# Kernel optimization log

Hardware: AMD Instinct MI355X
Metric: run time of the kernel (lower is better)

## Reference

```python
import jax, jax.numpy as jnp
import numpy as np

V, D, H, KH, FF, E = 50257, 512, 8, 64, 2048, 4
B, S = 8, 1024


def _glorot(key, shape):
    # VarianceScaling(1.0, 'fan_avg') with normal-ish draw
    fan_in, fan_out = shape[-2], shape[-1]
    scale = np.sqrt(2.0 / (fan_in + fan_out)).astype(np.float32)
    return jax.random.normal(key, shape, dtype=jnp.float32) * scale


def _mha(x, Wq, Wk, Wv, Wo):
    # haiku MultiHeadAttention (self-attn, no mask, zero biases at init)
    b, s, _ = x.shape
    q = (x @ Wq).reshape(b, s, H, KH)
    k = (x @ Wk).reshape(b, s, H, KH)
    v = (x @ Wv).reshape(b, s, H, KH)
    logits = jnp.einsum('bthd,bThd->bhtT', q, k) / jnp.asarray(np.sqrt(KH), x.dtype)
    attn = jax.nn.softmax(logits, axis=-1)
    o = jnp.einsum('bhtT,bThd->bthd', attn, v).reshape(b, s, H * KH)
    return o @ Wo


def setup_inputs() -> dict:
    key = jax.random.key(0)
    ks = jax.random.split(key, 16)
    tokens = jax.random.randint(ks[0], (B, S), 0, V, dtype=jnp.int32)
    emb = jax.random.normal(ks[1], (V, D), dtype=jnp.float32) * 0.02
    Wq = _glorot(ks[2], (D, H * KH))
    Wk = _glorot(ks[3], (D, H * KH))
    Wv = _glorot(ks[4], (D, H * KH))
    Wo = _glorot(ks[5], (H * KH, D))
    W1 = _glorot(ks[6], (D, FF))
    W2 = _glorot(ks[7], (FF, D))
    Wg = _glorot(ks[8], (D, E))
    eWq = _glorot(ks[9], (E, D, H * KH))
    eWk = _glorot(ks[10], (E, D, H * KH))
    eWv = _glorot(ks[11], (E, D, H * KH))
    eWo = _glorot(ks[12], (E, H * KH, D))
    eW1 = _glorot(ks[13], (E, D, FF))
    eW2 = _glorot(ks[14], (E, FF, D))
    Wout = _glorot(ks[15], (D, 1))
    return dict(tokens=tokens, emb=emb, Wq=Wq, Wk=Wk, Wv=Wv, Wo=Wo, W1=W1, W2=W2,
                Wg=Wg, eWq=eWq, eWk=eWk, eWv=eWv, eWo=eWo, eW1=eW1, eW2=eW2, Wout=Wout)


def reference(tokens, emb, Wq, Wk, Wv, Wo, W1, W2, Wg, eWq, eWk, eWv, eWo, eW1, eW2, Wout):
    x = emb[tokens]                                     # [B,S,D] embedding gather
    h = (_mha(x, Wq, Wk, Wv, Wo) @ W1) @ W2             # shared transformer block
    gate = h @ Wg                                       # [B,S,E]
    idx = jnp.argmax(gate, axis=-1)                     # [B,S] per-token expert id
    out = jnp.zeros_like(h)
    for e in range(E):                                  # naive masked dense dispatch
        mask = (idx == e)[..., None]                    # [B,S,1]
        xe = jnp.where(mask, h, 0.0)
        ye = (_mha(xe, eWq[e], eWk[e], eWv[e], eWo[e]) @ eW1[e]) @ eW2[e]
        out = out + ye                                  # sum-aggregate expert outputs
    return out @ Wout                                   # [B,S,1]
```

## Files before the change

kernel.cpp:

```cpp
#include <hip/hip_runtime.h>
#include <stdint.h>
#include <stddef.h>

typedef __bf16 bf16_8 __attribute__((ext_vector_type(8)));
typedef float  f32x4  __attribute__((ext_vector_type(4)));

__device__ __forceinline__ unsigned short f2bf(float f) {
    unsigned u = __float_as_uint(f);
    unsigned r = (u + 0x7fffu + ((u >> 16) & 1u)) >> 16;
    return (unsigned short)r;
}
__device__ __forceinline__ float bf2f(unsigned short s) {
    return __uint_as_float(((unsigned)s) << 16);
}
__device__ __forceinline__ void split3(float v, unsigned short& h, unsigned short& l, unsigned short& l2) {
    h = f2bf(v);
    float r1 = v - bf2f(h);
    l = f2bf(r1);
    l2 = f2bf(r1 - bf2f(l));
}
__device__ __forceinline__ void split2(float v, unsigned short& h, unsigned short& l) {
    h = f2bf(v);
    l = f2bf(v - bf2f(h));
}

template<int P>
__global__ __launch_bounds__(256)
void wsplit_kernel(const float* __restrict__ s0, const float* __restrict__ s1,
                   const float* __restrict__ s2, const float* __restrict__ s3,
                   unsigned short* __restrict__ d0, unsigned short* __restrict__ d1,
                   unsigned short* __restrict__ d2, unsigned short* __restrict__ d3,
                   int K, int N, int nper, size_t sstride, size_t dstride)
{
    const int z = blockIdx.z;
    const int arr = z / nper, e = z - arr * nper;
    const float* src = (arr == 0 ? s0 : arr == 1 ? s1 : arr == 2 ? s2 : s3) + (size_t)e * sstride;
    unsigned short* dst = (arr == 0 ? d0 : arr == 1 ? d1 : arr == 2 ? d2 : d3) + (size_t)e * dstride;
    const size_t NK = (size_t)N * K;
    __shared__ float T[64][65];
    const int n0 = blockIdx.x * 64, k0 = blockIdx.y * 64;
    const int tid = threadIdx.x;
#pragma unroll
    for (int i = 0; i < 16; ++i) {
        int idx = tid + (i << 8);
        int kk = idx >> 6, nn = idx & 63;
        T[kk][nn] = src[(size_t)(k0 + kk) * N + n0 + nn];
    }
    __syncthreads();
#pragma unroll
    for (int i = 0; i < 4; ++i) {
        int idx = (tid + (i << 8)) << 2;
        int nn = idx >> 6, kk = idx & 63;
        ushort4 hv, lv, l2v;
        unsigned short* hp = (unsigned short*)&hv;
        unsigned short* lp = (unsigned short*)&lv;
        unsigned short* l2p = (unsigned short*)&l2v;
#pragma unroll
        for (int j = 0; j < 4; ++j) {
            float v = T[kk + j][nn];
            unsigned short h = f2bf(v);
            hp[j] = h;
            if (P == 3) {
                float r1 = v - bf2f(h);
                unsigned short l = f2bf(r1);
                lp[j] = l;
                l2p[j] = f2bf(r1 - bf2f(l));
            }
        }
        unsigned short* dp = dst + (size_t)(n0 + nn) * K + k0 + kk;
        *(ushort4*)dp = hv;
        if (P == 3) {
            *(ushort4*)(dp + NK) = lv;
            *(ushort4*)(dp + 2 * NK) = l2v;
        }
    }
}

template<int TERMS, int AMODE, int CMODE, int NW, int BPRE, int A16, int C16>
__global__ __launch_bounds__(256, 2)
void gemm_kernel(const void* __restrict__ Av,
                 const void* __restrict__ B0, const void* __restrict__ B1, const void* __restrict__ B2,
                 void* __restrict__ C0, void* __restrict__ C1, void* __restrict__ C2,
                 int M, int N, int K,
                 size_t astride, size_t bstride, size_t cstride,
                 const int* __restrict__ OFF, const int* __restrict__ flat)
{
    const int z = blockIdx.z;
    const int e = z / NW, w = z - e * NW;
    int base = 0, cnt = M;
    if (AMODE == 1 || AMODE == 2 || CMODE == 1 || CMODE == 2) {
        base = OFF[e * 8];
        cnt  = OFF[e * 8 + 8] - base;
        if ((int)blockIdx.x * 128 >= cnt) return;
    }
    const void* Bsel = (NW == 3 ? (w == 0 ? B0 : w == 1 ? B1 : B2) : B0);
    void*       Csel = (NW == 3 ? (w == 0 ? C0 : w == 1 ? C1 : C2) : C0);
    const float*          Af = (const float*)Av + (size_t)e * astride;
    const unsigned short* As = (const unsigned short*)Av;
    const float*          Bf = (const float*)Bsel + (size_t)e * bstride;
    const unsigned short* Bp = (const unsigned short*)Bsel + (size_t)e * bstride;
    float*          Cf = (float*)Csel + (size_t)e * cstride;
    unsigned short* Cs = (unsigned short*)Csel + (size_t)e * cstride;
    const size_t NKb = (size_t)N * K;

    constexpr int NPL = (TERMS == 6) ? 3 : 1;
    __shared__ unsigned short Asm[NPL][128 * 40];
    __shared__ unsigned short Bsm[NPL][128 * 40];

    const int tid   = threadIdx.x;
    const int lane  = tid & 63;
    const int wid   = tid >> 6;
    const int wm    = wid & 1, wn = wid >> 1;
    const int mlane = lane & 15, quad = lane >> 4;
    const int row0  = blockIdx.x * 128;
    const int col0  = blockIdx.y * 128;

    f32x4 acc[4][4];
#pragma unroll
    for (int i = 0; i < 4; ++i)
#pragma unroll
        for (int j = 0; j < 4; ++j)
#pragma unroll
            for (int r = 0; r < 4; ++r) acc[i][j][r] = 0.f;

    for (int k0 = 0; k0 < K; k0 += 32) {
        if (A16 == 0) {
#pragma unroll
            for (int i = 0; i < 4; ++i) {
                int idx = tid + (i << 8);
                int r = idx >> 3;
                int c = (idx & 7) << 2;
                int lr = row0 + r;
                if (AMODE != 0) lr = min(lr, cnt - 1);
                size_t arow = (AMODE == 2) ? (size_t)flat[base + lr]
                            : (AMODE == 1) ? (size_t)(base + lr) : (size_t)lr;
                const float4 a = *(const float4*)(Af + arow * K + k0 + c);
                float av[4] = {a.x, a.y, a.z, a.w};
                ushort4 hv, lv, l2v;
                unsigned short* hp  = (unsigned short*)&hv;
                unsigned short* lp  = (unsigned short*)&lv;
                unsigned short* l2p = (unsigned short*)&l2v;
#pragma unroll
                for (int j = 0; j < 4; ++j) {
                    unsigned short h = f2bf(av[j]);
                    hp[j] = h;
                    if (TERMS == 6) {
                        float r1 = av[j] - bf2f(h);
                        unsigned short l = f2bf(r1);
                        lp[j]  = l;
                        l2p[j] = f2bf(r1 - bf2f(l));
                    }
                }
                *(ushort4*)&Asm[0][r * 40 + c] = hv;
                if (TERMS == 6) {
                    *(ushort4*)&Asm[1][r * 40 + c] = lv;
                    *(ushort4*)&Asm[2][r * 40 + c] = l2v;
                }
            }
        } else {
#pragma unroll
            for (int p = 0; p < NPL; ++p)
#pragma unroll
                for (int j = 0; j < 2; ++j) {
                    int c = tid * 2 + j;
                    int r = c >> 2, q8 = (c & 3) << 3;
                    int lr = row0 + r;
                    if (AMODE != 0) lr = min(lr, cnt - 1);
                    size_t arow = (AMODE == 2) ? (size_t)flat[base + lr]
                                : (AMODE == 1) ? (size_t)(base + lr) : (size_t)lr;
                    *(uint4*)&Asm[p][r * 40 + q8] =
                        *(const uint4*)(As + (size_t)p * astride + arow * K + k0 + q8);
                }
        }
        if (BPRE == 0) {
#pragma unroll
            for (int i = 0; i < 2; ++i) {
                int idx = tid + (i << 8);
                int kk = idx >> 4;
                int n8 = (idx & 15) << 3;
                const float* bp = Bf + (size_t)(k0 + kk) * N + col0 + n8;
                const float4 b0 = *(const float4*)bp;
                const float4 b1 = *(const float4*)(bp + 4);
                float bv[8] = {b0.x, b0.y, b0.z, b0.w, b1.x, b1.y, b1.z, b1.w};
#pragma unroll
                for (int j = 0; j < 8; ++j) {
                    unsigned short h = f2bf(bv[j]);
                    Bsm[0][(n8 + j) * 40 + kk] = h;
                    if (TERMS == 6) {
                        float r1 = bv[j] - bf2f(h);
                        unsigned short l = f2bf(r1);
                        Bsm[1][(n8 + j) * 40 + kk] = l;
                        Bsm[2][(n8 + j) * 40 + kk] = f2bf(r1 - bf2f(l));
                    }
                }
            }
        } else {
#pragma unroll
            for (int p = 0; p < NPL; ++p)
#pragma unroll
                for (int j = 0; j < 2; ++j) {
                    int c = tid * 2 + j;
                    int r = c >> 2, q8 = (c & 3) << 3;
                    *(uint4*)&Bsm[p][r * 40 + q8] =
                        *(const uint4*)(Bp + (size_t)p * NKb + (size_t)(col0 + r) * K + k0 + q8);
                }
        }
        __syncthreads();

        bf16_8 fa[3][4], fb[3][4];
#pragma unroll
        for (int t = 0; t < 4; ++t) {
            int ar = (wm * 64 + t * 16 + mlane) * 40 + quad * 8;
            int br = (wn * 64 + t * 16 + mlane) * 40 + quad * 8;
            fa[0][t] = *(const bf16_8*)&Asm[0][ar];
            fb[0][t] = *(const bf16_8*)&Bsm[0][br];
            if (TERMS == 6) {
                fa[1][t] = *(const bf16_8*)&Asm[1][ar];
                fa[2][t] = *(const bf16_8*)&Asm[2][ar];
                fb[1][t] = *(const bf16_8*)&Bsm[1][br];
                fb[2][t] = *(const bf16_8*)&Bsm[2][br];
            }
        }
        const int ta[6] = {0, 0, 1, 0, 1, 2};
        const int tb[6] = {0, 1, 0, 2, 1, 0};
#pragma unroll
        for (int s = 0; s < TERMS; ++s)
#pragma unroll
            for (int mt = 0; mt < 4; ++mt)
#pragma unroll
                for (int nt = 0; nt < 4; ++nt)
                    acc[mt][nt] = __builtin_amdgcn_mfma_f32_16x16x32_bf16(
                        fa[ta[s]][mt], fb[tb[s]][nt], acc[mt][nt], 0, 0, 0);
        __syncthreads();
    }

#pragma unroll
    for (int mt = 0; mt < 4; ++mt)
#pragma unroll
        for (int nt = 0; nt < 4; ++nt) {
            int c = col0 + wn * 64 + nt * 16 + mlane;
#pragma unroll
            for (int j = 0; j < 4; ++j) {
                int lr = row0 + wm * 64 + mt * 16 + quad * 4 + j;
                if ((CMODE == 1 || CMODE == 2) && lr >= cnt) continue;
                size_t crow = (CMODE == 2) ? (size_t)flat[base + lr]
                            : (CMODE == 1) ? (size_t)(base + lr) : (size_t)lr;
                if (C16) Cs[crow * N + c] = f2bf(acc[mt][nt][j]);
                else     Cf[crow * N + c] = acc[mt][nt][j];
            }
        }
}

__global__ __launch_bounds__(256)
void meanv_gemm_kernel(const float* __restrict__ in, const float* __restrict__ W,
                       float* __restrict__ out, int N, int K,
                       size_t instride, size_t wstride, size_t outstride)
{
    const int e  = blockIdx.z;
    const int nl = threadIdx.x & 63;
    const int kg = threadIdx.x >> 6;
    const int n  = blockIdx.x * 64 + nl;
    const int k0 = blockIdx.y * 512;

    const float* inp = in + (size_t)e * instride + k0;
    const float* wp  = W + (size_t)e * wstride + (size_t)(k0 + kg * 128) * N + n;

    __shared__ float mv[8][512];
    for (int i = threadIdx.x; i < 4096; i += 256) {
        int b = i >> 9, k = i & 511;
        mv[b][k] = inp[(size_t)b * K + k];
    }
    __syncthreads();

    float acc[8] = {0.f, 0.f, 0.f, 0.f, 0.f, 0.f, 0.f, 0.f};
#pragma unroll 8
    for (int k = 0; k < 128; ++k) {
        float wv = wp[(size_t)k * N];
        const float* mk = &mv[0][kg * 128 + k];
#pragma unroll
        for (int b = 0; b < 8; ++b) acc[b] += mk[b * 512] * wv;
    }

    __shared__ float red[4][8][64];
#pragma unroll
    for (int b = 0; b < 8; ++b) red[kg][b][nl] = acc[b];
    __syncthreads();
    if (kg == 0) {
        float* op = out + (size_t)e * outstride + n;
#pragma unroll
        for (int b = 0; b < 8; ++b) {
            float s = red[0][b][nl] + red[1][b][nl] + red[2][b][nl] + red[3][b][nl];
            if (gridDim.y == 1) op[(size_t)b * N] = s;
            else                atomicAdd(&op[(size_t)b * N], s);
        }
    }
}

__global__ __launch_bounds__(256, 2)
void attn_kernel(const float* __restrict__ Q, const float* __restrict__ Km,
                 const float* __restrict__ V, float* __restrict__ O)
{
    __shared__ __align__(16) unsigned short Ks[3][2][32][40];
    __shared__ __align__(16) unsigned short Vt[3][64][40];
    __shared__ __align__(16) unsigned short U[15360];

    const int tid = threadIdx.x;
    const int lane = tid & 63;
    const int w = tid >> 6;
    const int mlane = lane & 15, quad = lane >> 4;

    const int qt = blockIdx.x & 15;
    const int h  = (blockIdx.x >> 4) & 7;
    const int b  = blockIdx.x >> 7;
    const size_t rowbase = (size_t)b * 1024;
    const int colbase = h * 64;

#pragma unroll
    for (int i = 0; i < 4; ++i) {
        int idx = tid + (i << 8);
        int r = idx >> 4, c4 = (idx & 15) << 2;
        const float4 a = *(const float4*)(Q + (rowbase + qt * 64 + r) * 512 + colbase + c4);
        float av[4] = {a.x, a.y, a.z, a.w};
        ushort4 hv, lv, l2v;
        unsigned short* hp  = (unsigned short*)&hv;
        unsigned short* lp  = (unsigned short*)&lv;
        unsigned short* l2p = (unsigned short*)&l2v;
#pragma unroll
        for (int j = 0; j < 4; ++j) split3(av[j], hp[j], lp[j], l2p[j]);
        int ch = c4 >> 5, cm = c4 & 31;
        *(ushort4*)&U[(((0 * 2 + ch) * 64) + r) * 40 + cm] = hv;
        *(ushort4*)&U[(((1 * 2 + ch) * 64) + r) * 40 + cm] = lv;
        *(ushort4*)&U[(((2 * 2 + ch) * 64) + r) * 40 + cm] = l2v;
    }
    __syncthreads();

    bf16_8 fq[3][2];
#pragma unroll
    for (int p = 0; p < 3; ++p)
#pragma unroll
        for (int c = 0; c < 2; ++c)
            fq[p][c] = *(const bf16_8*)&U[(((p * 2 + c) * 64) + (w * 16 + mlane)) * 40 + quad * 8];
    __syncthreads();

    f32x4 oacc[4];
#pragma unroll
    for (int i = 0; i < 4; ++i)
#pragma unroll
        for (int j = 0; j < 4; ++j) oacc[i][j] = 0.f;
    float m_run = -1e30f, l_run = 0.f;

    const int ta[6] = {0, 0, 1, 0, 1, 2};
    const int tb[6] = {0, 1, 0, 2, 1, 0};

    for (int tt = 0; tt < 32; ++tt) {
        __syncthreads();
#pragma unroll
        for (int i = 0; i < 2; ++i) {
            int idx = tid + (i << 8);
            int r = idx >> 4, c4 = (idx & 15) << 2;
            const float4 a = *(const float4*)(Km + (rowbase + tt * 32 + r) * 512 + colbase + c4);
            float av[4] = {a.x, a.y, a.z, a.w};
            ushort4 hv, lv, l2v;
            unsigned short* hp  = (unsigned short*)&hv;
            unsigned short* lp  = (unsigned short*)&lv;
            unsigned short* l2p = (unsigned short*)&l2v;
#pragma unroll
            for (int j = 0; j < 4; ++j) split3(av[j], hp[j], lp[j], l2p[j]);
            int ch = c4 >> 5, cm = c4 & 31;
            *(ushort4*)&Ks[0][ch][r][cm] = hv;
            *(ushort4*)&Ks[1][ch][r][cm] = lv;
            *(ushort4*)&Ks[2][ch][r][cm] = l2v;
        }
#pragma unroll
        for (int i = 0; i < 2; ++i) {
            int idx = tid + (i << 8);
            int d = idx & 63, k4 = (idx >> 6) << 2;
            const float* vp = V + (rowbase + tt * 32 + k4) * 512 + colbase + d;
            float vv[4] = {vp[0], vp[512], vp[1024], vp[1536]};
            ushort4 hv, lv, l2v;
            unsigned short* hp  = (unsigned short*)&hv;
            unsigned short* lp  = (unsigned short*)&lv;
            unsigned short* l2p = (unsigned short*)&l2v;
#pragma unroll
            for (int j = 0; j < 4; ++j) split3(vv[j], hp[j], lp[j], l2p[j]);
            *(ushort4*)&Vt[0][d][k4] = hv;
            *(ushort4*)&Vt[1][d][k4] = lv;
            *(ushort4*)&Vt[2][d][k4] = l2v;
        }
        __syncthreads();

        f32x4 sacc[2];
#pragma unroll
        for (int mm = 0; mm < 2; ++mm)
#pragma unroll
            for (int j = 0; j < 4; ++j) sacc[mm][j] = 0.f;
        bf16_8 fk[3][2][2];
#pragma unroll
        for (int p = 0; p < 3; ++p)
#pragma unroll
            for (int c = 0; c < 2; ++c)
#pragma unroll
                for (int mm = 0; mm < 2; ++mm)
                    fk[p][c][mm] = *(const bf16_8*)&Ks[p][c][mm * 16 + mlane][quad * 8];
#pragma unroll
        for (int s = 0; s < 6; ++s)
#pragma unroll
            for (int c = 0; c < 2; ++c)
#pragma unroll
                for (int mm = 0; mm < 2; ++mm)
                    sacc[mm] = __builtin_amdgcn_mfma_f32_16x16x32_bf16(
                        fk[ta[s]][c][mm], fq[tb[s]][c], sacc[mm], 0, 0, 0);

        float sv[2][4];
#pragma unroll
        for (int mm = 0; mm < 2; ++mm)
#pragma unroll
            for (int j = 0; j < 4; ++j) sv[mm][j] = sacc[mm][j] * 0.125f;
        float tmax = sv[0][0];
#pragma unroll
        for (int mm = 0; mm < 2; ++mm)
#pragma unroll
            for (int j = 0; j < 4; ++j) tmax = fmaxf(tmax, sv[mm][j]);
        tmax = fmaxf(tmax, __shfl_xor(tmax, 16));
        tmax = fmaxf(tmax, __shfl_xor(tmax, 32));
        float mnew = fmaxf(m_run, tmax);
        float alpha = __expf(m_run - mnew);
        float lsum = 0.f;
#pragma unroll
        for (int mm = 0; mm < 2; ++mm)
#pragma unroll
            for (int j = 0; j < 4; ++j) {
                float p = __expf(sv[mm][j] - mnew);
                sv[mm][j] = p;
                lsum += p;
            }
        lsum += __shfl_xor(lsum, 16);
        lsum += __shfl_xor(lsum, 32);
        l_run = l_run * alpha + lsum;
        m_run = mnew;
#pragma unroll
        for (int mm = 0; mm < 4; ++mm)
#pragma unroll
            for (int j = 0; j < 4; ++j) oacc[mm][j] *= alpha;

#pragma unroll
        for (int mm = 0; mm < 2; ++mm) {
            ushort4 hv, lv, l2v;
            unsigned short* hp  = (unsigned short*)&hv;
            unsigned short* lp  = (unsigned short*)&lv;
            unsigned short* l2p = (unsigned short*)&l2v;
#pragma unroll
            for (int j = 0; j < 4; ++j) split3(sv[mm][j], hp[j], lp[j], l2p[j]);
            int col = mm * 16 + quad * 4;
            *(ushort4*)&U[((w * 3 + 0) * 16 + mlane) * 40 + col] = hv;
            *(ushort4*)&U[((w * 3 + 1) * 16 + mlane) * 40 + col] = lv;
            *(ushort4*)&U[((w * 3 + 2) * 16 + mlane) * 40 + col] = l2v;
        }

        bf16_8 fp[3], fv[3][4];
#pragma unroll
        for (int p = 0; p < 3; ++p) {
            fp[p] = *(const bf16_8*)&U[((w * 3 + p) * 16 + mlane) * 40 + quad * 8];
#pragma unroll
            for (int mm = 0; mm < 4; ++mm)
                fv[p][mm] = *(const bf16_8*)&Vt[p][mm * 16 + mlane][quad * 8];
        }
#pragma unroll
        for (int s = 0; s < 6; ++s)
#pragma unroll
            for (int mm = 0; mm < 4; ++mm)
                oacc[mm] = __builtin_amdgcn_mfma_f32_16x16x32_bf16(
                    fv[ta[s]][mm], fp[tb[s]], oacc[mm], 0, 0, 0);
    }

    const float inv = 1.f / l_run;
    const size_t orow = (rowbase + qt * 64 + w * 16 + mlane) * 512 + colbase;
#pragma unroll
    for (int mm = 0; mm < 4; ++mm)
#pragma unroll
        for (int j = 0; j < 4; ++j)
            O[orow + mm * 16 + quad * 4 + j] = oacc[mm][j] * inv;
}

__global__ __launch_bounds__(256, 3)
void attn_compact_kernel(const float* __restrict__ Qc, const float* __restrict__ Kc,
                         const float* __restrict__ Vc, const float* __restrict__ meanV,
                         unsigned short* __restrict__ AOc, const int* __restrict__ OFF)
{
    const int qt = blockIdx.x & 15;
    const int h  = (blockIdx.x >> 4) & 7;
    const int e  = (blockIdx.x >> 7) & 3;
    const int b  = blockIdx.x >> 9;
    const int base = OFF[e * 8 + b];
    const int c    = OFF[e * 8 + b + 1] - base;
    if (qt * 64 >= c) return;
    const int nq = min(64, c - qt * 64);

    __shared__ __align__(16) unsigned short Ks[2][2][32][40];
    __shared__ __align__(16) unsigned short Vt[2][64][40];
    __shared__ __align__(16) unsigned short U[10240];

    const int tid = threadIdx.x;
    const int lane = tid & 63;
    const int w = tid >> 6;
    const int mlane = lane & 15, quad = lane >> 4;
    const int colbase = h * 64;
    const int cmax = c - 1;

#pragma unroll
    for (int i = 0; i < 4; ++i) {
        int idx = tid + (i << 8);
        int r = idx >> 4, c4 = (idx & 15) << 2;
        const size_t g = (size_t)(base + min(qt * 64 + r, cmax)) * 512 + colbase + c4;
        const float4 a = *(const float4*)(Qc + g);
        float av[4] = {a.x, a.y, a.z, a.w};
        ushort4 hv, lv;
        unsigned short* hp = (unsigned short*)&hv;
        unsigned short* lp = (unsigned short*)&lv;
#pragma unroll
        for (int j = 0; j < 4; ++j) split2(av[j], hp[j], lp[j]);
        int ch = c4 >> 5, cm = c4 & 31;
        *(ushort4*)&U[(((0 * 2 + ch) * 64) + r) * 40 + cm] = hv;
        *(ushort4*)&U[(((1 * 2 + ch) * 64) + r) * 40 + cm] = lv;
    }
    __syncthreads();

    bf16_8 fq[2][2];
#pragma unroll
    for (int p = 0; p < 2; ++p)
#pragma unroll
        for (int cc = 0; cc < 2; ++cc)
            fq[p][cc] = *(const bf16_8*)&U[(((p * 2 + cc) * 64) + (w * 16 + mlane)) * 40 + quad * 8];
    __syncthreads();

    f32x4 oacc[4];
#pragma unroll
    for (int i = 0; i < 4; ++i)
#pragma unroll
        for (int j = 0; j < 4; ++j) oacc[i][j] = 0.f;
    float m_run = -1e30f, l_run = 0.f;

    const int ta3[3] = {0, 0, 1};
    const int tb3[3] = {0, 1, 0};

    for (int kt = 0; kt * 32 < c; ++kt) {
        __syncthreads();
#pragma unroll
        for (int i = 0; i < 2; ++i) {
            int idx = tid + (i << 8);
            int r = idx >> 4, c4 = (idx & 15) << 2;
            const size_t g = (size_t)(base + min(kt * 32 + r, cmax)) * 512 + colbase + c4;
            const float4 a = *(const float4*)(Kc + g);
            float av[4] = {a.x, a.y, a.z, a.w};
            ushort4 hv, lv;
            unsigned short* hp = (unsigned short*)&hv;
            unsigned short* lp = (unsigned short*)&lv;
#pragma unroll
            for (int j = 0; j < 4; ++j) split2(av[j], hp[j], lp[j]);
            int ch = c4 >> 5, cm = c4 & 31;
            *(ushort4*)&Ks[0][ch][r][cm] = hv;
            *(ushort4*)&Ks[1][ch][r][cm] = lv;
        }
#pragma unroll
        for (int i = 0; i < 2; ++i) {
            int idx = tid + (i << 8);
            int d = idx & 63, k4 = (idx >> 6) << 2;
            float vv[4];
#pragma unroll
            for (int j = 0; j < 4; ++j)
                vv[j] = Vc[(size_t)(base + min(kt * 32 + k4 + j, cmax)) * 512 + colbase + d];
            ushort4 hv, lv;
            unsigned short* hp = (unsigned short*)&hv;
            unsigned short* lp = (unsigned short*)&lv;
#pragma unroll
            for (int j = 0; j < 4; ++j) split2(vv[j], hp[j], lp[j]);
            *(ushort4*)&Vt[0][d][k4] = hv;
            *(ushort4*)&Vt[1][d][k4] = lv;
        }
        __syncthreads();

        f32x4 sacc[2];
#pragma unroll
        for (int mm = 0; mm < 2; ++mm)
#pragma unroll
            for (int j = 0; j < 4; ++j) sacc[mm][j] = 0.f;
        bf16_8 fk[2][2][2];
#pragma unroll
        for (int p = 0; p < 2; ++p)
#pragma unroll
            for (int cc = 0; cc < 2; ++cc)
#pragma unroll
                for (int mm = 0; mm < 2; ++mm)
                    fk[p][cc][mm] = *(const bf16_8*)&Ks[p][cc][mm * 16 + mlane][quad * 8];
#pragma unroll
        for (int s = 0; s < 3; ++s)
#pragma unroll
            for (int cc = 0; cc < 2; ++cc)
#pragma unroll
                for (int mm = 0; mm < 2; ++mm)
                    sacc[mm] = __builtin_amdgcn_mfma_f32_16x16x32_bf16(
                        fk[ta3[s]][cc][mm], fq[tb3[s]][cc], sacc[mm], 0, 0, 0);

        float sv[2][4];
#pragma unroll
        for (int mm = 0; mm < 2; ++mm)
#pragma unroll
            for (int j = 0; j < 4; ++j) {
                int kg = kt * 32 + mm * 16 + quad * 4 + j;
                sv[mm][j] = (kg < c) ? sacc[mm][j] * 0.125f : -1e30f;
            }
        float tmax = sv[0][0];
#pragma unroll
        for (int mm = 0; mm < 2; ++mm)
#pragma unroll
            for (int j = 0; j < 4; ++j) tmax = fmaxf(tmax, sv[mm][j]);
        tmax = fmaxf(tmax, __shfl_xor(tmax, 16));
        tmax = fmaxf(tmax, __shfl_xor(tmax, 32));
        float mnew = fmaxf(m_run, tmax);
        float alpha = __expf(m_run - mnew);
        float lsum = 0.f;
#pragma unroll
        for (int mm = 0; mm < 2; ++mm)
#pragma unroll
            for (int j = 0; j < 4; ++j) {
                float p = __expf(sv[mm][j] - mnew);
                sv[mm][j] = p;
                lsum += p;
            }
        lsum += __shfl_xor(lsum, 16);
        lsum += __shfl_xor(lsum, 32);
        l_run = l_run * alpha + lsum;
        m_run = mnew;
#pragma unroll
        for (int mm = 0; mm < 4; ++mm)
#pragma unroll
            for (int j = 0; j < 4; ++j) oacc[mm][j] *= alpha;

#pragma unroll
        for (int mm = 0; mm < 2; ++mm) {
            ushort4 hv, lv;
            unsigned short* hp = (unsigned short*)&hv;
            unsigned short* lp = (unsigned short*)&lv;
#pragma unroll
            for (int j = 0; j < 4; ++j) split2(sv[mm][j], hp[j], lp[j]);
            int col = mm * 16 + quad * 4;
            *(ushort4*)&U[((w * 2 + 0) * 16 + mlane) * 40 + col] = hv;
            *(ushort4*)&U[((w * 2 + 1) * 16 + mlane) * 40 + col] = lv;
        }

        bf16_8 fp[2], fv[2][4];
#pragma unroll
        for (int p = 0; p < 2; ++p) {
            fp[p] = *(const bf16_8*)&U[((w * 2 + p) * 16 + mlane) * 40 + quad * 8];
#pragma unroll
            for (int mm = 0; mm < 4; ++mm)
                fv[p][mm] = *(const bf16_8*)&Vt[p][mm * 16 + mlane][quad * 8];
        }
#pragma unroll
        for (int s = 0; s < 3; ++s)
#pragma unroll
            for (int mm = 0; mm < 4; ++mm)
                oacc[mm] = __builtin_amdgcn_mfma_f32_16x16x32_bf16(
                    fv[ta3[s]][mm], fp[tb3[s]], oacc[mm], 0, 0, 0);
    }

    float mfin = (c < 1024) ? fmaxf(m_run, 0.f) : m_run;
    float alphaf = __expf(m_run - mfin);
    l_run = l_run * alphaf + (float)(1024 - c) * __expf(-mfin);
#pragma unroll
    for (int mm = 0; mm < 4; ++mm)
#pragma unroll
        for (int j = 0; j < 4; ++j) oacc[mm][j] *= alphaf;

    const int qi = w * 16 + mlane;
    if (qi < nq) {
        const float inv = 1.f / l_run;
        const size_t orow = (size_t)(base + qt * 64 + qi) * 512 + colbase;
        const float* mv = meanV + e * 65536 + b * 512 + colbase;
#pragma unroll
        for (int mm = 0; mm < 4; ++mm) {
            int d0 = mm * 16 + quad * 4;
            ushort4 o;
            o.x = f2bf(oacc[mm][0] * inv - mv[d0 + 0]);
            o.y = f2bf(oacc[mm][1] * inv - mv[d0 + 1]);
            o.z = f2bf(oacc[mm][2] * inv - mv[d0 + 2]);
            o.w = f2bf(oacc[mm][3] * inv - mv[d0 + 3]);
            *(ushort4*)&AOc[orow + d0] = o;
        }
    }
}

__global__ void sumv_kernel(const float* __restrict__ Vc, const int* __restrict__ OFF,
                            float* __restrict__ M32)
{
    const int h = blockIdx.x & 7, e = (blockIdx.x >> 3) & 3, b = blockIdx.x >> 5;
    const int base = OFF[e * 8 + b], c = OFF[e * 8 + b + 1] - base;
    const int tid = threadIdx.x;
    const int d = tid & 63, g = tid >> 6;
    float s = 0.f;
    for (int r = g; r < c; r += 4) s += Vc[(size_t)(base + r) * 512 + h * 64 + d];
    __shared__ float red[256];
    red[tid] = s;
    __syncthreads();
    if (g == 0)
        M32[e * 65536 + b * 512 + h * 64 + d] =
            (red[d] + red[64 + d] + red[128 + d] + red[192 + d]) * (1.f / 1024.f);
}

__global__ void gather_kernel(const int* __restrict__ tokens,
                              const float* __restrict__ emb,
                              unsigned short* __restrict__ Xp)
{
    const int t = blockIdx.x;
    const int tok = tokens[t];
    const int d4 = threadIdx.x * 4;
    const float4 a = *(const float4*)(emb + (size_t)tok * 512 + d4);
    float av[4] = {a.x, a.y, a.z, a.w};
    ushort4 hv, lv, l2v;
    unsigned short* hp  = (unsigned short*)&hv;
    unsigned short* lp  = (unsigned short*)&lv;
    unsigned short* l2p = (unsigned short*)&l2v;
#pragma unroll
    for (int j = 0; j < 4; ++j) split3(av[j], hp[j], lp[j], l2p[j]);
    const size_t o = (size_t)t * 512 + d4;
    *(ushort4*)&Xp[o]           = hv;
    *(ushort4*)&Xp[o + 4194304] = lv;
    *(ushort4*)&Xp[o + 8388608] = l2v;
}

__global__ __launch_bounds__(256)
void gate_kernel(const float* __restrict__ H, const float* __restrict__ Wg,
                 int* __restrict__ idx)
{
    const int t = blockIdx.x * 4 + (threadIdx.x >> 6);
    const int lane = threadIdx.x & 63;
    float a0 = 0, a1 = 0, a2 = 0, a3 = 0;
#pragma unroll
    for (int i = 0; i < 8; ++i) {
        int d = i * 64 + lane;
        float hv = H[(size_t)t * 512 + d];
        a0 += hv * Wg[d * 4 + 0];
        a1 += hv * Wg[d * 4 + 1];
        a2 += hv * Wg[d * 4 + 2];
        a3 += hv * Wg[d * 4 + 3];
    }
#pragma unroll
    for (int off = 32; off > 0; off >>= 1) {
        a0 += __shfl_down(a0, off);
        a1 += __shfl_down(a1, off);
        a2 += __shfl_down(a2, off);
        a3 += __shfl_down(a3, off);
    }
    if (lane == 0) {
        int best = 0; float bv = a0;
        if (a1 > bv) { bv = a1; best = 1; }
        if (a2 > bv) { bv = a2; best = 2; }
        if (a3 > bv) { bv = a3; best = 3; }
        idx[t] = best;
    }
}

__global__ void count_kernel(const int* __restrict__ idx, int* __restrict__ cnt)
{
    const int t = blockIdx.x * 256 + threadIdx.x;
    atomicAdd(&cnt[idx[t] * 8 + (t >> 10)], 1);
}
__global__ void offsets_kernel(const int* __restrict__ cnt, int* __restrict__ OFF,
                               int* __restrict__ cursor)
{
    if (threadIdx.x == 0) {
        int a = 0;
        for (int i = 0; i < 32; ++i) { OFF[i] = a; cursor[i] = a; a += cnt[i]; }
        OFF[32] = a;
    }
}
__global__ void fill_kernel(const int* __restrict__ idx, int* __restrict__ cursor,
                            int* __restrict__ flat)
{
    const int t = blockIdx.x * 256 + threadIdx.x;
    const int p = atomicAdd(&cursor[idx[t] * 8 + (t >> 10)], 1);
    flat[p] = t;
}

__global__ void sb_kernel(const float* __restrict__ G2, const float* __restrict__ Wout,
                          float* __restrict__ SB)
{
    const int tid = threadIdx.x;
    const int pair = tid >> 3, t8 = tid & 7;
    const int e = pair >> 3, b = pair & 7;
    float s = 0.f;
    for (int d = t8; d < 512; d += 8) s += G2[e * 65536 + b * 512 + d] * Wout[d];
    __shared__ float red[256];
    __shared__ float red2[32];
    red[tid] = s;
    __syncthreads();
    if (tid < 32) {
        float t = 0.f;
#pragma unroll
        for (int k = 0; k < 8; ++k) t += red[tid * 8 + k];
        red2[tid] = t;
    }
    __syncthreads();
    if (tid < 8)
        SB[tid] = red2[tid] + red2[8 + tid] + red2[16 + tid] + red2[24 + tid];
}

__global__ __launch_bounds__(256)
void wout_kernel(const float* __restrict__ OUT, const float* __restrict__ Wout,
                 const float* __restrict__ SB, float* __restrict__ out)
{
    const int t = blockIdx.x * 4 + (threadIdx.x >> 6);
    const int lane = threadIdx.x & 63;
    float s = 0.f;
#pragma unroll
    for (int i = 0; i < 8; ++i) {
        int d = i * 64 + lane;
        s += OUT[(size_t)t * 512 + d] * Wout[d];
    }
#pragma unroll
    for (int off = 32; off > 0; off >>= 1) s += __shfl_down(s, off);
    if (lane == 0) out[t] = s + SB[t >> 10];
}

extern "C" void kernel_launch(void* const* d_in, const int* in_sizes, int n_in,
                              void* d_out, int out_size, void* d_ws, size_t ws_size,
                              hipStream_t stream)
{
    const int*   tokens = (const int*)d_in[0];
    const float* emb  = (const float*)d_in[1];
    const float* Wq   = (const float*)d_in[2];
    const float* Wk   = (const float*)d_in[3];
    const float* Wv   = (const float*)d_in[4];
    const float* Wo   = (const float*)d_in[5];
    const float* W1   = (const float*)d_in[6];
    const float* W2   = (const float*)d_in[7];
    const float* Wg   = (const float*)d_in[8];
    const float* eWq  = (const float*)d_in[9];
    const float* eWk  = (const float*)d_in[10];
    const float* eWv  = (const float*)d_in[11];
    const float* eWo  = (const float*)d_in[12];
    const float* eW1  = (const float*)d_in[13];
    const float* eW2  = (const float*)d_in[14];
    const float* Wout = (const float*)d_in[15];
    float* outp = (float*)d_out;

    float* WS = (float*)d_ws;
    const size_t SZ = (size_t)8192 * 512;
    float* P0 = WS, *P1 = WS + SZ, *P2 = WS + 2 * SZ, *P3 = WS + 3 * SZ, *P4 = WS + 4 * SZ;

    unsigned short* SP   = (unsigned short*)(WS + 5 * SZ);
    unsigned short* sW1p = SP;
    unsigned short* sW2p = SP + 3145728;
    unsigned short* xWq  = SP + 6291456;
    unsigned short* xWk  = xWq + 1048576;
    unsigned short* xWv  = xWk + 1048576;
    unsigned short* xWo  = xWv + 1048576;
    unsigned short* xW1  = xWo + 1048576;
    unsigned short* xW2  = xW1 + 4194304;

    float* MBase = WS + 5 * SZ + 9437184;
    int* IDX    = (int*)MBase;
    int* cnt    = (int*)(MBase + 8192);
    int* OFFp   = (int*)(MBase + 8224);
    int* cursor = (int*)(MBase + 8264);
    int* flat   = (int*)(MBase + 8304);
    float* M32  = MBase + 16640;
    float* G0   = M32 + 262144;
    float* G2   = G0 + 262144;
    float* SB   = G2 + 262144;

    float* Qb = P0, *Kb = P1, *Vb = P2, *AO = P3, *T0 = P4, *T1 = P0, *Hb = P4;
    unsigned short* Xp = (unsigned short*)P3;
    float* Qc = P0, *Kc = P1, *Vc = P2;
    unsigned short* AOc = (unsigned short*)P3;
    unsigned short* T0c = (unsigned short*)(P3 + 2097152);
    unsigned short* T1c = (unsigned short*)P0;
    float* G1 = P2;
    float* OA = P3;

    const int M = 8192, D = 512, FF = 2048;
    const size_t sDD = (size_t)D * D, sDF = (size_t)D * FF;
    const float* NUL = nullptr;
    float* NULm = nullptr;

    wsplit_kernel<3><<<dim3(32, 8, 1),  256, 0, stream>>>(W1, NUL, NUL, NUL, sW1p, 0, 0, 0, D, FF, 1, 0, 0);
    wsplit_kernel<3><<<dim3(8, 32, 1),  256, 0, stream>>>(W2, NUL, NUL, NUL, sW2p, 0, 0, 0, FF, D, 1, 0, 0);
    wsplit_kernel<3><<<dim3(8, 8, 4),   256, 0, stream>>>(Wq, Wk, Wv, Wo, xWq, xWk, xWv, xWo, D, D, 1, 0, 0);
    wsplit_kernel<1><<<dim3(32, 8, 4),  256, 0, stream>>>(eW1, NUL, NUL, NUL, xW1, 0, 0, 0, D, FF, 4, sDF, 1048576);
    wsplit_kernel<1><<<dim3(8, 32, 4),  256, 0, stream>>>(eW2, NUL, NUL, NUL, xW2, 0, 0, 0, FF, D, 4, sDF, 1048576);

    gather_kernel<<<8192, 128, 0, stream>>>(tokens, emb, Xp);
    gemm_kernel<6, 0, 0, 3, 1, 1, 0><<<dim3(64, 4, 3), 256, 0, stream>>>(
        Xp, xWq, xWk, xWv, Qb, Kb, Vb, M, D, D, (size_t)M * D, 0, 0, nullptr, nullptr);
    attn_kernel<<<1024, 256, 0, stream>>>(Qb, Kb, Vb, AO);
    gemm_kernel<6, 0, 0, 1, 1, 0, 0><<<dim3(64, 4, 1), 256, 0, stream>>>(
        AO, xWo, NUL, NUL, T0, NULm, NULm, M, D, D, 0, 0, 0, nullptr, nullptr);
    wsplit_kernel<1><<<dim3(8, 8, 16),  256, 0, stream>>>(eWq, eWk, eWv, eWo, xWq, xWk, xWv, xWo, D, D, 4, sDD, 262144);
    gemm_kernel<6, 0, 0, 1, 1, 0, 0><<<dim3(64, 16, 1), 256, 0, stream>>>(
        T0, sW1p, NUL, NUL, T1, NULm, NULm, M, FF, D, 0, 0, 0, nullptr, nullptr);
    gemm_kernel<6, 0, 0, 1, 1, 0, 0><<<dim3(64, 4, 1), 256, 0, stream>>>(
        T1, sW2p, NUL, NUL, Hb, NULm, NULm, M, D, FF, 0, 0, 0, nullptr, nullptr);
    gate_kernel<<<2048, 256, 0, stream>>>(Hb, Wg, IDX);

    hipMemsetAsync(cnt, 0, 32 * sizeof(int), stream);
    hipMemsetAsync(M32, 0, 4 * 128 * 512 * sizeof(float), stream);
    hipMemsetAsync(G2, 0, 262144 * sizeof(float), stream);
    count_kernel<<<32, 256, 0, stream>>>(IDX, cnt);
    offsets_kernel<<<1, 64, 0, stream>>>(cnt, OFFp, cursor);
    fill_kernel<<<32, 256, 0, stream>>>(IDX, cursor, flat);

    gemm_kernel<1, 2, 1, 3, 1, 0, 0><<<dim3(64, 4, 12), 256, 0, stream>>>(
        Hb, xWq, xWk, xWv, Qc, Kc, Vc, M, D, D, 0, 262144, 0, OFFp, flat);
    sumv_kernel<<<256, 256, 0, stream>>>(Vc, OFFp, M32);
    attn_compact_kernel<<<4096, 256, 0, stream>>>(Qc, Kc, Vc, M32, AOc, OFFp);

    gemm_kernel<1, 1, 1, 1, 1, 1, 1><<<dim3(64, 4, 4), 256, 0, stream>>>(
        AOc, xWo, NUL, NUL, T0c, NULm, NULm, M, D, D, 0, 262144, 0, OFFp, flat);
    gemm_kernel<1, 1, 1, 1, 1, 1, 1><<<dim3(64, 16, 4), 256, 0, stream>>>(
        T0c, xW1, NUL, NUL, T1c, NULm, NULm, M, FF, D, 0, 1048576, 0, OFFp, flat);

    meanv_gemm_kernel<<<dim3(8, 1, 4),  256, 0, stream>>>(M32, eWo, G0, 512,  512,  65536,  sDD, 65536);
    meanv_gemm_kernel<<<dim3(32, 1, 4), 256, 0, stream>>>(G0,  eW1, G1, 2048, 512,  65536,  sDF, 262144);
    meanv_gemm_kernel<<<dim3(8, 4, 4),  256, 0, stream>>>(G1,  eW2, G2, 512,  2048, 262144, sDF, 65536);

    gemm_kernel<1, 1, 2, 1, 1, 1, 0><<<dim3(64, 4, 4), 256, 0, stream>>>(
        T1c, xW2, NUL, NUL, OA, NULm, NULm, M, D, FF, 0, 1048576, 0, OFFp, flat);

    sb_kernel<<<1, 256, 0, stream>>>(G2, Wout, SB);
    wout_kernel<<<2048, 256, 0, stream>>>(OA, Wout, SB, outp);
}
```

Baseline: 1.384 ms.

## Emit pre-split bf16 K/V planes from GEMM epilogues instead of splitting in attention

The Q/K/V projection GEMMs are split into separate launches, and the K and V ones now write bf16 hi/lo(/lo2) planes directly in their epilogue (new C16 modes 2 and 3). The attention kernels then load ready-made bf16 planes into shared memory and no longer run the split arithmetic once per query-tile block. This removes the redundant split work repeated across query tiles. In exchange it costs three GEMM launches instead of one, more global bytes per plane, and strided 16-bit V loads. Some weight-split launches are also moved later in the sequence.

```diff
diff --git a/kernel.cpp b/kernel.cpp
--- a/kernel.cpp
+++ b/kernel.cpp
@@ -101,6 +101,7 @@
     const unsigned short* Bp = (const unsigned short*)Bsel + (size_t)e * bstride;
     float*          Cf = (float*)Csel + (size_t)e * cstride;
     unsigned short* Cs = (unsigned short*)Csel + (size_t)e * cstride;
+    unsigned short* Cp = (unsigned short*)Csel;
     const size_t NKb = (size_t)N * K;
 
     constexpr int NPL = (TERMS == 6) ? 3 : 1;
@@ -245,8 +246,20 @@
                 if ((CMODE == 1 || CMODE == 2) && lr >= cnt) continue;
                 size_t crow = (CMODE == 2) ? (size_t)flat[base + lr]
                             : (CMODE == 1) ? (size_t)(base + lr) : (size_t)lr;
-                if (C16) Cs[crow * N + c] = f2bf(acc[mt][nt][j]);
-                else     Cf[crow * N + c] = acc[mt][nt][j];
+                size_t o = crow * N + c;
+                if (C16 == 2) {
+                    unsigned short h, l, l2;
+                    split3(acc[mt][nt][j], h, l, l2);
+                    Cp[o] = h; Cp[cstride + o] = l; Cp[2 * cstride + o] = l2;
+                } else if (C16 == 3) {
+                    unsigned short h, l;
+                    split2(acc[mt][nt][j], h, l);
+                    Cp[o] = h; Cp[cstride + o] = l;
+                } else if (C16 == 1) {
+                    Cs[o] = f2bf(acc[mt][nt][j]);
+                } else {
+                    Cf[o] = acc[mt][nt][j];
+                }
             }
         }
 }
@@ -297,8 +310,8 @@
 }
 
 __global__ __launch_bounds__(256, 2)
-void attn_kernel(const float* __restrict__ Q, const float* __restrict__ Km,
-                 const float* __restrict__ V, float* __restrict__ O)
+void attn_kernel(const float* __restrict__ Q, const unsigned short* __restrict__ Kp,
+                 const unsigned short* __restrict__ Vp, float* __restrict__ O)
 {
     __shared__ __align__(16) unsigned short Ks[3][2][32][40];
     __shared__ __align__(16) unsigned short Vt[3][64][40];
@@ -352,40 +365,29 @@
     const int ta[6] = {0, 0, 1, 0, 1, 2};
     const int tb[6] = {0, 1, 0, 2, 1, 0};
 
+    const int kr = tid >> 3, kc8 = (tid & 7) << 3;
+    const int kch = kc8 >> 5, kcm = kc8 & 31;
+
     for (int tt = 0; tt < 32; ++tt) {
         __syncthreads();
+        {
+            const size_t g = (rowbase + tt * 32 + kr) * 512 + colbase + kc8;
+#pragma unroll
+            for (int p = 0; p < 3; ++p)
+                *(uint4*)&Ks[p][kch][kr][kcm] = *(const uint4*)(Kp + (size_t)p * 4194304 + g);
+        }
 #pragma unroll
         for (int i = 0; i < 2; ++i) {
             int idx = tid + (i << 8);
-            int r = idx >> 4, c4 = (idx & 15) << 2;
-            const float4 a = *(const float4*)(Km + (rowbase + tt * 32 + r) * 512 + colbase + c4);
-            float av[4] = {a.x, a.y, a.z, a.w};
-            ushort4 hv, lv, l2v;
-            unsigned short* hp  = (unsigned short*)&hv;
-            unsigned short* lp  = (unsigned short*)&lv;
-            unsigned short* l2p = (unsigned short*)&l2v;
-#pragma unroll
-            for (int j = 0; j < 4; ++j) split3(av[j], hp[j], lp[j], l2p[j]);
-            int ch = c4 >> 5, cm = c4 & 31;
-            *(ushort4*)&Ks[0][ch][r][cm] = hv;
-            *(ushort4*)&Ks[1][ch][r][cm] = lv;
-            *(ushort4*)&Ks[2][ch][r][cm] = l2v;
-        }
-#pragma unroll
-        for (int i = 0; i < 2; ++i) {
-            int idx = tid + (i << 8);
-            int d = idx & 63, k4 = (idx >> 6) << 2;
-            const float* vp = V + (rowbase + tt * 32 + k4) * 512 + colbase + d;
-            float vv[4] = {vp[0], vp[512], vp[1024], vp[1536]};
-            ushort4 hv, lv, l2v;
-            unsigned short* hp  = (unsigned short*)&hv;
-            unsigned short* lp  = (unsigned short*)&lv;
-            unsigned short* l2p = (unsigned short*)&l2v;
-#pragma unroll
-            for (int j = 0; j < 4; ++j) split3(vv[j], hp[j], lp[j], l2p[j]);
-            *(ushort4*)&Vt[0][d][k4] = hv;
-            *(ushort4*)&Vt[1][d][k4] = lv;
-            *(ushort4*)&Vt[2][d][k4] = l2v;
+            int vd = idx & 63, vk4 = (idx >> 6) << 2;
+            const size_t g = (rowbase + tt * 32 + vk4) * 512 + colbase + vd;
+#pragma unroll
+            for (int p = 0; p < 3; ++p) {
+                const unsigned short* vp = Vp + (size_t)p * 16777216 + g;
+                ushort4 vv;
+                vv.x = vp[0]; vv.y = vp[512]; vv.z = vp[1024]; vv.w = vp[1536];
+                *(ushort4*)&Vt[p][vd][vk4] = vv;
+            }
         }
         __syncthreads();
 
@@ -483,8 +485,8 @@
 }
 
 __global__ __launch_bounds__(256, 3)
-void attn_compact_kernel(const float* __restrict__ Qc, const float* __restrict__ Kc,
-                         const float* __restrict__ Vc, const float* __restrict__ meanV,
+void attn_compact_kernel(const float* __restrict__ Qc, const unsigned short* __restrict__ Kc,
+                         const unsigned short* __restrict__ Vc, const float* __restrict__ meanV,
                          unsigned short* __restrict__ AOc, const int* __restrict__ OFF)
 {
     const int qt = blockIdx.x & 15;
@@ -543,39 +545,31 @@
     const int ta3[3] = {0, 0, 1};
     const int tb3[3] = {0, 1, 0};
 
+    const int kr = tid >> 3, kc8 = (tid & 7) << 3;
+    const int kch = kc8 >> 5, kcm = kc8 & 31;
+
     for (int kt = 0; kt * 32 < c; ++kt) {
         __syncthreads();
+        {
+            const size_t g = (size_t)(base + min(kt * 32 + kr, cmax)) * 512 + colbase + kc8;
+#pragma unroll
+            for (int p = 0; p < 2; ++p)
+                *(uint4*)&Ks[p][kch][kr][kcm] = *(const uint4*)(Kc + (size_t)p * 4194304 + g);
+        }
 #pragma unroll
         for (int i = 0; i < 2; ++i) {
             int idx = tid + (i << 8);
-            int r = idx >> 4, c4 = (idx & 15) << 2;
-            const size_t g = (size_t)(base + min(kt * 32 + r, cmax)) * 512 + colbase + c4;
-            const float4 a = *(const float4*)(Kc + g);
-            float av[4] = {a.x, a.y, a.z, a.w};
-            ushort4 hv, lv;
-            unsigned short* hp = (unsigned short*)&hv;
-            unsigned short* lp = (unsigned short*)&lv;
-#pragma unroll
-            for (int j = 0; j < 4; ++j) split2(av[j], hp[j], lp[j]);
-            int ch = c4 >> 5, cm = c4 & 31;
-            *(ushort4*)&Ks[0][ch][r][cm] = hv;
-            *(ushort4*)&Ks[1][ch][r][cm] = lv;
-        }
-#pragma unroll
-        for (int i = 0; i < 2; ++i) {
-            int idx = tid + (i << 8);
-            int d = idx & 63, k4 = (idx >> 6) << 2;
-            float vv[4];
-#pragma unroll
-            for (int j = 0; j < 4; ++j)
-                vv[j] = Vc[(size_t)(base + min(kt * 32 + k4 + j, cmax)) * 512 + colbase + d];
-            ushort4 hv, lv;
-            unsigned short* hp = (unsigned short*)&hv;
-            unsigned short* lp = (unsigned short*)&lv;
-#pragma unroll
-            for (int j = 0; j < 4; ++j) split2(vv[j], hp[j], lp[j]);
-            *(ushort4*)&Vt[0][d][k4] = hv;
-            *(ushort4*)&Vt[1][d][k4] = lv;
+            int vd = idx & 63, vk4 = (idx >> 6) << 2;
+#pragma unroll
+            for (int p = 0; p < 2; ++p) {
+                const unsigned short* vb = Vc + (size_t)p * 4194304 + colbase + vd;
+                ushort4 vv;
+                vv.x = vb[(size_t)(base + min(kt * 32 + vk4 + 0, cmax)) * 512];
+                vv.y = vb[(size_t)(base + min(kt * 32 + vk4 + 1, cmax)) * 512];
+                vv.z = vb[(size_t)(base + min(kt * 32 + vk4 + 2, cmax)) * 512];
+                vv.w = vb[(size_t)(base + min(kt * 32 + vk4 + 3, cmax)) * 512];
+                *(ushort4*)&Vt[p][vd][vk4] = vv;
+            }
         }
         __syncthreads();
 
@@ -690,7 +684,7 @@
     }
 }
 
-__global__ void sumv_kernel(const float* __restrict__ Vc, const int* __restrict__ OFF,
+__global__ void sumv_kernel(const unsigned short* __restrict__ Vc, const int* __restrict__ OFF,
                             float* __restrict__ M32)
 {
     const int h = blockIdx.x & 7, e = (blockIdx.x >> 3) & 3, b = blockIdx.x >> 5;
@@ -698,7 +692,10 @@
     const int tid = threadIdx.x;
     const int d = tid & 63, g = tid >> 6;
     float s = 0.f;
-    for (int r = g; r < c; r += 4) s += Vc[(size_t)(base + r) * 512 + h * 64 + d];
+    for (int r = g; r < c; r += 4) {
+        const unsigned short* vp = Vc + (size_t)(base + r) * 512 + h * 64 + d;
+        s += bf2f(vp[0]) + bf2f(vp[4194304]);
+    }
     __shared__ float red[256];
     red[tid] = s;
     __syncthreads();
@@ -869,9 +866,13 @@
     float* G2   = G0 + 262144;
     float* SB   = G2 + 262144;
 
-    float* Qb = P0, *Kb = P1, *Vb = P2, *AO = P3, *T0 = P4, *T1 = P0, *Hb = P4;
-    unsigned short* Xp = (unsigned short*)P3;
-    float* Qc = P0, *Kc = P1, *Vc = P2;
+    float* Qb = P0, *AO = P3, *T0 = P4, *T1 = P0, *Hb = P4;
+    unsigned short* Xp  = (unsigned short*)P3;
+    unsigned short* Kpp = (unsigned short*)P1;
+    unsigned short* Vpp = (unsigned short*)(WS + 10485760);
+    float* Qc = P0;
+    unsigned short* KcP = (unsigned short*)P1;
+    unsigned short* VcP = (unsigned short*)P2;
     unsigned short* AOc = (unsigned short*)P3;
     unsigned short* T0c = (unsigned short*)(P3 + 2097152);
     unsigned short* T1c = (unsigned short*)P0;
@@ -886,16 +887,20 @@
     wsplit_kernel<3><<<dim3(32, 8, 1),  256, 0, stream>>>(W1, NUL, NUL, NUL, sW1p, 0, 0, 0, D, FF, 1, 0, 0);
     wsplit_kernel<3><<<dim3(8, 32, 1),  256, 0, stream>>>(W2, NUL, NUL, NUL, sW2p, 0, 0, 0, FF, D, 1, 0, 0);
     wsplit_kernel<3><<<dim3(8, 8, 4),   256, 0, stream>>>(Wq, Wk, Wv, Wo, xWq, xWk, xWv, xWo, D, D, 1, 0, 0);
-    wsplit_kernel<1><<<dim3(32, 8, 4),  256, 0, stream>>>(eW1, NUL, NUL, NUL, xW1, 0, 0, 0, D, FF, 4, sDF, 1048576);
-    wsplit_kernel<1><<<dim3(8, 32, 4),  256, 0, stream>>>(eW2, NUL, NUL, NUL, xW2, 0, 0, 0, FF, D, 4, sDF, 1048576);
 
     gather_kernel<<<8192, 128, 0, stream>>>(tokens, emb, Xp);
-    gemm_kernel<6, 0, 0, 3, 1, 1, 0><<<dim3(64, 4, 3), 256, 0, stream>>>(
-        Xp, xWq, xWk, xWv, Qb, Kb, Vb, M, D, D, (size_t)M * D, 0, 0, nullptr, nullptr);
-    attn_kernel<<<1024, 256, 0, stream>>>(Qb, Kb, Vb, AO);
+    gemm_kernel<6, 0, 0, 1, 1, 1, 0><<<dim3(64, 4, 1), 256, 0, stream>>>(
+        Xp, xWq, NUL, NUL, Qb, NULm, NULm, M, D, D, (size_t)M * D, 0, 0, nullptr, nullptr);
+    gemm_kernel<6, 0, 0, 1, 1, 1, 2><<<dim3(64, 4, 1), 256, 0, stream>>>(
+        Xp, xWk, NUL, NUL, Kpp, NULm, NULm, M, D, D, (size_t)M * D, 0, 4194304, nullptr, nullptr);
+    gemm_kernel<6, 0, 0, 1, 1, 1, 2><<<dim3(64, 4, 1), 256, 0, stream>>>(
+        Xp, xWv, NUL, NUL, Vpp, NULm, NULm, M, D, D, (size_t)M * D, 0, 16777216, nullptr, nullptr);
+    attn_kernel<<<1024, 256, 0, stream>>>(Qb, Kpp, Vpp, AO);
     gemm_kernel<6, 0, 0, 1, 1, 0, 0><<<dim3(64, 4, 1), 256, 0, stream>>>(
         AO, xWo, NUL, NUL, T0, NULm, NULm, M, D, D, 0, 0, 0, nullptr, nullptr);
     wsplit_kernel<1><<<dim3(8, 8, 16),  256, 0, stream>>>(eWq, eWk, eWv, eWo, xWq, xWk, xWv, xWo, D, D, 4, sDD, 262144);
+    wsplit_kernel<1><<<dim3(32, 8, 4),  256, 0, stream>>>(eW1, NUL, NUL, NUL, xW1, 0, 0, 0, D, FF, 4, sDF, 1048576);
+    wsplit_kernel<1><<<dim3(8, 32, 4),  256, 0, stream>>>(eW2, NUL, NUL, NUL, xW2, 0, 0, 0, FF, D, 4, sDF, 1048576);
     gemm_kernel<6, 0, 0, 1, 1, 0, 0><<<dim3(64, 16, 1), 256, 0, stream>>>(
         T0, sW1p, NUL, NUL, T1, NULm, NULm, M, FF, D, 0, 0, 0, nullptr, nullptr);
     gemm_kernel<6, 0, 0, 1, 1, 0, 0><<<dim3(64, 4, 1), 256, 0, stream>>>(
@@ -909,10 +914,14 @@
     offsets_kernel<<<1, 64, 0, stream>>>(cnt, OFFp, cursor);
     fill_kernel<<<32, 256, 0, stream>>>(IDX, cursor, flat);
 
-    gemm_kernel<1, 2, 1, 3, 1, 0, 0><<<dim3(64, 4, 12), 256, 0, stream>>>(
-        Hb, xWq, xWk, xWv, Qc, Kc, Vc, M, D, D, 0, 262144, 0, OFFp, flat);
-    sumv_kernel<<<256, 256, 0, stream>>>(Vc, OFFp, M32);
-    attn_compact_kernel<<<4096, 256, 0, stream>>>(Qc, Kc, Vc, M32, AOc, OFFp);
+    gemm_kernel<1, 2, 1, 1, 1, 0, 0><<<dim3(64, 4, 4), 256, 0, stream>>>(
+        Hb, xWq, NUL, NUL, Qc, NULm, NULm, M, D, D, 0, 262144, 0, OFFp, flat);
+    gemm_kernel<1, 2, 1, 1, 1, 0, 3><<<dim3(64, 4, 4), 256, 0, stream>>>(
+        Hb, xWk, NUL, NUL, KcP, NULm, NULm, M, D, D, 0, 262144, 4194304, OFFp, flat);
+    gemm_kernel<1, 2, 1, 1, 1, 0, 3><<<dim3(64, 4, 4), 256, 0, stream>>>(
+        Hb, xWv, NUL, NUL, VcP, NULm, NULm, M, D, D, 0, 262144, 4194304, OFFp, flat);
+    sumv_kernel<<<256, 256, 0, stream>>>(VcP, OFFp, M32);
+    attn_compact_kernel<<<4096, 256, 0, stream>>>(Qc, KcP, VcP, M32, AOc, OFFp);
 
     gemm_kernel<1, 1, 1, 1, 1, 1, 1><<<dim3(64, 4, 4), 256, 0, stream>>>(
         AOc, xWo, NUL, NUL, T0c, NULm, NULm, M, D, D, 0, 262144, 0, OFFp, flat);
```

Result: slower. 1.446 ms (+4.5%).
